# Optimization experiments

Hardware: AMD Instinct MI355X
Metric: run time of the kernel (lower is better)

Reference implementation:

```python
import jax, jax.numpy as jnp
import numpy as np
from jax.scipy.special import logsumexp

TEMPERATURE = 0.05
HARD_NEG_WEIGHT = 1.0
MARGIN = 0.2
EXPLICIT_NEG_WEIGHT = 2.0
NEG_INF = -1e9


def setup_inputs() -> dict:
    key = jax.random.key(0)
    k1, k2, k3 = jax.random.split(key, 3)
    N, D = 8192, 512
    return {
        "asm_embeddings": jax.random.normal(k1, (N, D), dtype=jnp.float32),
        "source_embeddings": jax.random.normal(k2, (N, D), dtype=jnp.float32),
        "labels": jax.random.randint(k3, (N,), 0, 2, dtype=jnp.int64),
    }


def reference(asm_embeddings, source_embeddings, labels):
    # L2-normalize both embedding sets
    a = asm_embeddings / jnp.linalg.norm(asm_embeddings, axis=1, keepdims=True)
    s = source_embeddings / jnp.linalg.norm(source_embeddings, axis=1, keepdims=True)
    sim = jnp.matmul(a, s.T) / TEMPERATURE  # [N, N]

    N = labels.shape[0]
    pos_mask = labels == 1
    neg_mask = labels == 0
    num_pos = jnp.sum(pos_mask).astype(sim.dtype)
    num_neg = jnp.sum(neg_mask)

    # column weights: explicit negatives (label==0) get EXPLICIT_NEG_WEIGHT,
    # others 1; the positive (diagonal) logit always has weight 1.
    log_w = jnp.log(jnp.where(neg_mask, EXPLICIT_NEG_WEIGHT, 1.0).astype(sim.dtype))
    eye = jnp.eye(N, dtype=bool)
    weighted_logits = sim + jnp.where(eye, 0.0, log_w[None, :])  # [N, N]

    lse = logsumexp(weighted_logits, axis=1)  # weighted logsumexp per row
    diag = jnp.diagonal(sim)
    per_row_loss = lse - diag  # -log_prob_pos

    infonce = jnp.sum(jnp.where(pos_mask, per_row_loss, 0.0)) / num_pos

    # margin penalty on hardest explicit-negative diagonal similarity
    mean_pos_sim = jnp.sum(jnp.where(pos_mask, diag, 0.0)) / num_pos
    hard_neg_sim = jnp.max(jnp.where(neg_mask, diag, NEG_INF))
    penalty = jax.nn.relu(hard_neg_sim - mean_pos_sim + MARGIN)
    penalty = jnp.where(num_neg > 0, penalty, 0.0)

    return infonce + HARD_NEG_WEIGHT * penalty
```

## Files before the change

kernel.cpp:

```cpp
#include <hip/hip_runtime.h>
#include <math.h>

#define NROWS 8192
#define DIM 512
#define INV_T 20.0f
#define QS 500.0f
#define DEQ2 (INV_T * 1.4426950408889634f / (QS * QS))

typedef __attribute__((ext_vector_type(4))) int i32x4;

__device__ __forceinline__ void gload_lds16(const void* g, void* l) {
    __builtin_amdgcn_global_load_lds(
        (const __attribute__((address_space(1))) unsigned int*)g,
        (__attribute__((address_space(3))) unsigned int*)l, 16, 0, 0);
}

__device__ __forceinline__ float hw_exp2(float x) {
    float r;
    asm("v_exp_f32 %0, %1" : "=v"(r) : "v"(x));
    return r;
}

__device__ __forceinline__ float dot4(float4 a, float4 b) {
    return a.x * b.x + a.y * b.y + a.z * b.z + a.w * b.w;
}

__device__ __forceinline__ int q4(float4 v, float s) {
    int b0 = __float2int_rn(fminf(fmaxf(v.x * s, -127.f), 127.f)) & 255;
    int b1 = __float2int_rn(fminf(fmaxf(v.y * s, -127.f), 127.f)) & 255;
    int b2 = __float2int_rn(fminf(fmaxf(v.z * s, -127.f), 127.f)) & 255;
    int b3 = __float2int_rn(fminf(fmaxf(v.w * s, -127.f), 127.f)) & 255;
    return b0 | (b1 << 8) | (b2 << 16) | (b3 << 24);
}

__global__ __launch_bounds__(256) void norm_kernel(
    const float* __restrict__ A, const float* __restrict__ S,
    const int* __restrict__ labels, signed char* __restrict__ aQ,
    signed char* __restrict__ sQ, float* __restrict__ diag,
    float* __restrict__ lw2, float* __restrict__ lsum) {
    const int wave = threadIdx.x >> 6, lane = threadIdx.x & 63;
    const int row = blockIdx.x * 4 + wave;
    const float4* a4 = (const float4*)(A + (size_t)row * DIM);
    const float4* s4 = (const float4*)(S + (size_t)row * DIM);
    float4 a0 = a4[lane], a1 = a4[lane + 64];
    float4 s0 = s4[lane], s1 = s4[lane + 64];
    float saa = dot4(a0, a0) + dot4(a1, a1);
    float sss = dot4(s0, s0) + dot4(s1, s1);
    float sas = dot4(a0, s0) + dot4(a1, s1);
    for (int m = 1; m < 64; m <<= 1) {
        saa += __shfl_xor(saa, m);
        sss += __shfl_xor(sss, m);
        sas += __shfl_xor(sas, m);
    }
    const float ra = rsqrtf(saa), rs = rsqrtf(sss);
    signed char* arow = aQ + (size_t)row * DIM;
    signed char* srow = sQ + (size_t)row * DIM;
    *(int*)(arow + lane * 4)       = q4(a0, ra * QS);
    *(int*)(arow + 256 + lane * 4) = q4(a1, ra * QS);
    *(int*)(srow + lane * 4)       = q4(s0, rs * QS);
    *(int*)(srow + 256 + lane * 4) = q4(s1, rs * QS);
    if (lane == 0) {
        diag[row] = sas * ra * rs * INV_T;
        lw2[row] = (labels[row] == 0) ? 1.0f : 0.0f;
        lsum[row] = 0.0f;
    }
}

__global__ __launch_bounds__(512, 4) void lse_gemm(
    const signed char* __restrict__ Aq, const signed char* __restrict__ Bq,
    const float* __restrict__ lw2, float* __restrict__ lsum) {
    __shared__ __align__(16) char lds[49152];

    const int bid = blockIdx.x;
    const int xcd = bid & 7, idx = bid >> 3;
    const int rt = (xcd >> 1) * 8 + (idx & 7);
    const int ctg = (xcd & 1) * 8 + (idx >> 3);
    const int row0 = rt * 256;
    const int colg = ctg * 512;

    const int tid = threadIdx.x;
    const int wid = tid >> 6, lane = tid & 63;
    const int wr = wid >> 1, wc = wid & 1;
    const int fr = lane & 15, grp = lane >> 4;

    const int sl = (tid & 3) ^ ((tid >> 3) & 3);
    const signed char* aSrc = Aq + (size_t)(row0 + (tid >> 2)) * DIM + sl * 16;
    const signed char* bSrc = Bq + (size_t)(colg + (tid >> 2)) * DIM + sl * 16;
    char* dstA = lds + tid * 16;
    char* dstB = lds + 16384 + tid * 16;

#define STAGE(buf, TT)                                                        \
    do {                                                                      \
        const int ct_ = (TT) >> 3, k_ = (TT) & 7;                             \
        gload_lds16(aSrc + k_ * 64,               dstA + (buf) * 24576);      \
        gload_lds16(aSrc + 65536 + k_ * 64,       dstA + (buf) * 24576 + 8192); \
        gload_lds16(bSrc + ct_ * 65536 + k_ * 64, dstB + (buf) * 24576);      \
    } while (0)

    const int ps = (grp ^ ((fr >> 1) & 3)) << 4;
    const char* rdA = lds + (wr * 64 + fr) * 64 + ps;
    const char* rdB = lds + 16384 + (wc * 64 + fr) * 64 + ps;

    STAGE(0, 0);

    i32x4 acc[4][4] = {};
#pragma unroll 2
    for (int T = 0; T < 32; ++T) {
        const int buf = T & 1;
        if (T < 31) {
            STAGE(buf ^ 1, T + 1);
            asm volatile("s_waitcnt vmcnt(3)" ::: "memory");
        } else {
            asm volatile("s_waitcnt vmcnt(0)" ::: "memory");
        }
        __builtin_amdgcn_s_barrier();

        i32x4 a[4], b[4];
#pragma unroll
        for (int m = 0; m < 4; ++m)
            a[m] = *(const i32x4*)(rdA + buf * 24576 + m * 1024);
#pragma unroll
        for (int n = 0; n < 4; ++n)
            b[n] = *(const i32x4*)(rdB + buf * 24576 + n * 1024);
        asm volatile("s_waitcnt lgkmcnt(0)" ::: "memory");
        __builtin_amdgcn_sched_barrier(0);

        __builtin_amdgcn_s_setprio(1);
#pragma unroll
        for (int m = 0; m < 4; ++m)
#pragma unroll
            for (int n = 0; n < 4; ++n)
                acc[m][n] = __builtin_amdgcn_mfma_i32_16x16x64_i8(
                    a[m], b[n], acc[m][n], 0, 0, 0);
        __builtin_amdgcn_s_setprio(0);

        if ((T & 7) == 7) {
            const int ct = T >> 3;
            const int col0 = colg + ct * 128 + wc * 64;
            float lwv[4];
#pragma unroll
            for (int n = 0; n < 4; ++n)
                lwv[n] = lw2[col0 + n * 16 + fr];
#pragma unroll
            for (int m = 0; m < 4; ++m)
#pragma unroll
                for (int j = 0; j < 4; ++j) {
                    float s = 0.f;
#pragma unroll
                    for (int n = 0; n < 4; ++n)
                        s += hw_exp2(fmaf((float)acc[m][n][j], DEQ2, lwv[n]));
                    s += __shfl_xor(s, 1);
                    s += __shfl_xor(s, 2);
                    s += __shfl_xor(s, 4);
                    s += __shfl_xor(s, 8);
                    if (fr == 0)
                        atomicAdd(&lsum[row0 + wr * 64 + m * 16 + grp * 4 + j], s);
                }
#pragma unroll
            for (int m = 0; m < 4; ++m)
#pragma unroll
                for (int n = 0; n < 4; ++n)
                    acc[m][n] = i32x4{0, 0, 0, 0};
        }
        __builtin_amdgcn_s_barrier();
    }
#undef STAGE
}

__global__ __launch_bounds__(1024) void finalize_kernel(
    const float* __restrict__ lsum, const float* __restrict__ diag,
    const int* __restrict__ labels, float* __restrict__ out) {
    const int tid = threadIdx.x;
    float sl = 0.f, sd = 0.f, mx = -1e9f;
    int np_ = 0, nn_ = 0;
#pragma unroll
    for (int i = tid; i < NROWS; i += 1024) {
        const float dg = diag[i];
        if (labels[i] == 1) {
            sl += logf(lsum[i]) - dg;
            sd += dg;
            np_++;
        } else {
            nn_++;
            mx = fmaxf(mx, dg);
        }
    }
    for (int m = 1; m < 64; m <<= 1) {
        sl += __shfl_xor(sl, m);
        sd += __shfl_xor(sd, m);
        mx = fmaxf(mx, __shfl_xor(mx, m));
        np_ += __shfl_xor(np_, m);
        nn_ += __shfl_xor(nn_, m);
    }
    __shared__ float rsl[16], rsd[16], rmx[16];
    __shared__ int rnp[16], rnn[16];
    const int wave = tid >> 6, lane = tid & 63;
    if (lane == 0) {
        rsl[wave] = sl; rsd[wave] = sd; rmx[wave] = mx;
        rnp[wave] = np_; rnn[wave] = nn_;
    }
    __syncthreads();
    if (tid == 0) {
        float SL = 0.f, SD = 0.f, MX = -1e9f;
        int NP = 0, NN = 0;
        for (int w = 0; w < 16; w++) {
            SL += rsl[w]; SD += rsd[w]; MX = fmaxf(MX, rmx[w]);
            NP += rnp[w]; NN += rnn[w];
        }
        const float infonce = SL / (float)NP;
        const float meanpos = SD / (float)NP;
        float pen = fmaxf(MX - meanpos + 0.2f, 0.0f);
        if (NN == 0) pen = 0.0f;
        out[0] = infonce + pen;
    }
}

extern "C" void kernel_launch(void* const* d_in, const int* in_sizes, int n_in,
                              void* d_out, int out_size, void* d_ws, size_t ws_size,
                              hipStream_t stream) {
    const float* A = (const float*)d_in[0];
    const float* S = (const float*)d_in[1];
    const int* labels = (const int*)d_in[2];
    float* out = (float*)d_out;

    char* ws = (char*)d_ws;
    signed char* aQ = (signed char*)ws;
    signed char* sQ = (signed char*)(ws + (size_t)NROWS * DIM);
    char* p = ws + (size_t)NROWS * DIM * 2;
    float* diag = (float*)p;
    float* lw2 = (float*)(p + 32768);
    float* lsum = (float*)(p + 65536);

    norm_kernel<<<NROWS / 4, 256, 0, stream>>>(A, S, labels, aQ, sQ, diag, lw2, lsum);
    lse_gemm<<<512, 512, 0, stream>>>(aQ, sQ, lw2, lsum);
    finalize_kernel<<<1, 1024, 0, stream>>>(lsum, diag, labels, out);
}
```

Before: 68.04 us.

## Compact positive-label rows and compute GEMM logsumexp only for them

Adds a single-block compaction kernel that builds a permutation of rows with label 1, and the GEMM now gathers only those rows, with blocks beyond the needed row-tile count exiting early. Only positive rows contribute to the loss, so this skips the GEMM and exp work for roughly half the rows. The cost is an extra kernel launch, a serial single-block scan, gathered A-row loads, and the loss of the previous XCD-aware block mapping. The finalize kernel reads the compacted sums through the permutation.

```diff
diff --git a/kernel.cpp b/kernel.cpp
--- a/kernel.cpp
+++ b/kernel.cpp
@@ -13,6 +13,12 @@
     __builtin_amdgcn_global_load_lds(
         (const __attribute__((address_space(1))) unsigned int*)g,
         (__attribute__((address_space(3))) unsigned int*)l, 16, 0, 0);
+}
+
+__device__ __forceinline__ void block_bar() {
+    asm volatile("" ::: "memory");
+    __builtin_amdgcn_s_barrier();
+    asm volatile("" ::: "memory");
 }
 
 __device__ __forceinline__ float hw_exp2(float x) {
@@ -37,7 +43,7 @@
     const float* __restrict__ A, const float* __restrict__ S,
     const int* __restrict__ labels, signed char* __restrict__ aQ,
     signed char* __restrict__ sQ, float* __restrict__ diag,
-    float* __restrict__ lw2, float* __restrict__ lsum) {
+    float* __restrict__ lw2) {
     const int wave = threadIdx.x >> 6, lane = threadIdx.x & 63;
     const int row = blockIdx.x * 4 + wave;
     const float4* a4 = (const float4*)(A + (size_t)row * DIM);
@@ -62,19 +68,57 @@
     if (lane == 0) {
         diag[row] = sas * ra * rs * INV_T;
         lw2[row] = (labels[row] == 0) ? 1.0f : 0.0f;
-        lsum[row] = 0.0f;
+    }
+}
+
+__global__ __launch_bounds__(1024) void compact_kernel(
+    const int* __restrict__ labels, int* __restrict__ perm,
+    float* __restrict__ lsum, int* __restrict__ meta) {
+    const int tid = threadIdx.x;
+    for (int i = tid; i < 8448; i += 1024) {
+        perm[i] = 0;
+        lsum[i] = 0.f;
+    }
+    __syncthreads();
+    const int lane = tid & 63, wid = tid >> 6;
+    int lab[8], cnt = 0;
+#pragma unroll
+    for (int i = 0; i < 8; ++i) {
+        lab[i] = labels[tid * 8 + i];
+        cnt += (lab[i] == 1);
+    }
+    int inc = cnt;
+    for (int d = 1; d < 64; d <<= 1) {
+        int v = __shfl_up(inc, d);
+        if (lane >= d) inc += v;
+    }
+    __shared__ int wsum[16], wpre[16];
+    if (lane == 63) wsum[wid] = inc;
+    __syncthreads();
+    if (tid == 0) {
+        int acc = 0;
+        for (int w = 0; w < 16; ++w) { acc += wsum[w]; wpre[w] = acc; }
+    }
+    __syncthreads();
+    int off = (wid ? wpre[wid - 1] : 0) + inc - cnt;
+#pragma unroll
+    for (int i = 0; i < 8; ++i)
+        if (lab[i] == 1) perm[off++] = tid * 8 + i;
+    if (tid == 0) {
+        meta[0] = wpre[15];
+        meta[1] = (wpre[15] + 255) >> 8;
     }
 }
 
 __global__ __launch_bounds__(512, 4) void lse_gemm(
     const signed char* __restrict__ Aq, const signed char* __restrict__ Bq,
-    const float* __restrict__ lw2, float* __restrict__ lsum) {
+    const float* __restrict__ lw2, const int* __restrict__ perm,
+    const int* __restrict__ meta, float* __restrict__ lsum) {
     __shared__ __align__(16) char lds[49152];
 
     const int bid = blockIdx.x;
-    const int xcd = bid & 7, idx = bid >> 3;
-    const int rt = (xcd >> 1) * 8 + (idx & 7);
-    const int ctg = (xcd & 1) * 8 + (idx >> 3);
+    const int rt = bid >> 4, ctg = bid & 15;
+    if (rt >= meta[1]) return;
     const int row0 = rt * 256;
     const int colg = ctg * 512;
 
@@ -84,7 +128,10 @@
     const int fr = lane & 15, grp = lane >> 4;
 
     const int sl = (tid & 3) ^ ((tid >> 3) & 3);
-    const signed char* aSrc = Aq + (size_t)(row0 + (tid >> 2)) * DIM + sl * 16;
+    const int r0 = perm[row0 + (tid >> 2)];
+    const int r1 = perm[row0 + 128 + (tid >> 2)];
+    const signed char* aSrc0 = Aq + (size_t)r0 * DIM + sl * 16;
+    const signed char* aSrc1 = Aq + (size_t)r1 * DIM + sl * 16;
     const signed char* bSrc = Bq + (size_t)(colg + (tid >> 2)) * DIM + sl * 16;
     char* dstA = lds + tid * 16;
     char* dstB = lds + 16384 + tid * 16;
@@ -92,8 +139,8 @@
 #define STAGE(buf, TT)                                                        \
     do {                                                                      \
         const int ct_ = (TT) >> 3, k_ = (TT) & 7;                             \
-        gload_lds16(aSrc + k_ * 64,               dstA + (buf) * 24576);      \
-        gload_lds16(aSrc + 65536 + k_ * 64,       dstA + (buf) * 24576 + 8192); \
+        gload_lds16(aSrc0 + k_ * 64,              dstA + (buf) * 24576);      \
+        gload_lds16(aSrc1 + k_ * 64,              dstA + (buf) * 24576 + 8192); \
         gload_lds16(bSrc + ct_ * 65536 + k_ * 64, dstB + (buf) * 24576);      \
     } while (0)
 
@@ -113,7 +160,7 @@
         } else {
             asm volatile("s_waitcnt vmcnt(0)" ::: "memory");
         }
-        __builtin_amdgcn_s_barrier();
+        block_bar();
 
         i32x4 a[4], b[4];
 #pragma unroll
@@ -162,53 +209,52 @@
                 for (int n = 0; n < 4; ++n)
                     acc[m][n] = i32x4{0, 0, 0, 0};
         }
-        __builtin_amdgcn_s_barrier();
+        block_bar();
     }
 #undef STAGE
 }
 
 __global__ __launch_bounds__(1024) void finalize_kernel(
     const float* __restrict__ lsum, const float* __restrict__ diag,
-    const int* __restrict__ labels, float* __restrict__ out) {
+    const int* __restrict__ labels, const int* __restrict__ perm,
+    const int* __restrict__ meta, float* __restrict__ out) {
     const int tid = threadIdx.x;
+    const int npos = meta[0];
     float sl = 0.f, sd = 0.f, mx = -1e9f;
-    int np_ = 0, nn_ = 0;
-#pragma unroll
+    int nn_ = 0;
+    for (int c = tid; c < npos; c += 1024) {
+        const int r = perm[c];
+        const float dg = diag[r];
+        sl += logf(lsum[c]) - dg;
+        sd += dg;
+    }
     for (int i = tid; i < NROWS; i += 1024) {
-        const float dg = diag[i];
-        if (labels[i] == 1) {
-            sl += logf(lsum[i]) - dg;
-            sd += dg;
-            np_++;
-        } else {
+        if (labels[i] == 0) {
             nn_++;
-            mx = fmaxf(mx, dg);
+            mx = fmaxf(mx, diag[i]);
         }
     }
     for (int m = 1; m < 64; m <<= 1) {
         sl += __shfl_xor(sl, m);
         sd += __shfl_xor(sd, m);
         mx = fmaxf(mx, __shfl_xor(mx, m));
-        np_ += __shfl_xor(np_, m);
         nn_ += __shfl_xor(nn_, m);
     }
     __shared__ float rsl[16], rsd[16], rmx[16];
-    __shared__ int rnp[16], rnn[16];
+    __shared__ int rnn[16];
     const int wave = tid >> 6, lane = tid & 63;
     if (lane == 0) {
-        rsl[wave] = sl; rsd[wave] = sd; rmx[wave] = mx;
-        rnp[wave] = np_; rnn[wave] = nn_;
+        rsl[wave] = sl; rsd[wave] = sd; rmx[wave] = mx; rnn[wave] = nn_;
     }
     __syncthreads();
     if (tid == 0) {
         float SL = 0.f, SD = 0.f, MX = -1e9f;
-        int NP = 0, NN = 0;
+        int NN = 0;
         for (int w = 0; w < 16; w++) {
-            SL += rsl[w]; SD += rsd[w]; MX = fmaxf(MX, rmx[w]);
-            NP += rnp[w]; NN += rnn[w];
-        }
-        const float infonce = SL / (float)NP;
-        const float meanpos = SD / (float)NP;
+            SL += rsl[w]; SD += rsd[w]; MX = fmaxf(MX, rmx[w]); NN += rnn[w];
+        }
+        const float infonce = SL / (float)npos;
+        const float meanpos = SD / (float)npos;
         float pen = fmaxf(MX - meanpos + 0.2f, 0.0f);
         if (NN == 0) pen = 0.0f;
         out[0] = infonce + pen;
@@ -230,8 +276,11 @@
     float* diag = (float*)p;
     float* lw2 = (float*)(p + 32768);
     float* lsum = (float*)(p + 65536);
-
-    norm_kernel<<<NROWS / 4, 256, 0, stream>>>(A, S, labels, aQ, sQ, diag, lw2, lsum);
-    lse_gemm<<<512, 512, 0, stream>>>(aQ, sQ, lw2, lsum);
-    finalize_kernel<<<1, 1024, 0, stream>>>(lsum, diag, labels, out);
-}
+    int* perm = (int*)(p + 65536 + 36864);
+    int* meta = (int*)(p + 65536 + 73728);
+
+    norm_kernel<<<NROWS / 4, 256, 0, stream>>>(A, S, labels, aQ, sQ, diag, lw2);
+    compact_kernel<<<1, 1024, 0, stream>>>(labels, perm, lsum, meta);
+    lse_gemm<<<512, 512, 0, stream>>>(aQ, sQ, lw2, perm, meta, lsum);
+    finalize_kernel<<<1, 1024, 0, stream>>>(lsum, diag, labels, perm, meta, out);
+}
```

Result: faster. 56.31 us, median of 2 (-17.2%).
